# Optimization experiments

Measured on AMD Instinct MI355X. Metric: run time of the kernel, lower is better.

The kernel has to match this reference:

```python
import jax, jax.numpy as jnp
import numpy as np

B, T, D = 2, 4096, 1024
H, L = 8, 2
DH = D // H           # 128
BS = 64               # bucket_size (lucidrains default)
NH = 8                # n_hashes (lucidrains default)
NB = T // BS          # 64 buckets (even, required)
FF = 4 * D


def setup_inputs() -> dict:
    key = jax.random.key(0)
    ks = jax.random.split(key, 16)
    s = 0.02
    return {
        'x': jax.random.normal(ks[0], (B, T, D), jnp.float32),
        'Wqk': jax.random.normal(ks[1], (L, D, H * DH), jnp.float32) * s,
        'Wv': jax.random.normal(ks[2], (L, D, H * DH), jnp.float32) * s,
        'Wout': jax.random.normal(ks[3], (L, H * DH, D), jnp.float32) * s,
        'bout': jnp.zeros((L, D), jnp.float32),
        'ln1_g': jnp.ones((L, D), jnp.float32),
        'ln1_b': jnp.zeros((L, D), jnp.float32),
        'W1': jax.random.normal(ks[4], (L, D, FF), jnp.float32) * s,
        'b1': jnp.zeros((L, FF), jnp.float32),
        'W2': jax.random.normal(ks[5], (L, FF, D), jnp.float32) * s,
        'b2': jnp.zeros((L, D), jnp.float32),
        'ln2_g': jnp.ones((L, D), jnp.float32),
        'ln2_b': jnp.zeros((L, D), jnp.float32),
        'rotations': jax.random.normal(ks[6], (L, DH, NH, NB // 2), jnp.float32),
    }


def _layer_norm(x, g, b):
    m = jnp.mean(x, axis=-1, keepdims=True)
    v = jnp.var(x, axis=-1, keepdims=True)
    return (x - m) * jax.lax.rsqrt(v + 1e-5) * g + b


def _look_one_back(x):
    # concat each chunk with the previous chunk (wrap-around), along the within-chunk axis
    return jnp.concatenate([x, jnp.roll(x, 1, axis=1)], axis=2)


def _lsh_attention(qk, v, rot):
    # qk, v: (bh, T, DH); rot: (DH, NH, NB//2). Causal LSH attention (lucidrains defaults).
    bh, t, d = qk.shape
    rotated = jnp.einsum('btd,dhr->bhtr', qk, rot)
    rotated = jnp.concatenate([rotated, -rotated], axis=-1)          # (bh, NH, T, NB)
    buckets = jnp.argmax(rotated, axis=-1)                            # (bh, NH, T)
    buckets = buckets + (jnp.arange(NH) * NB)[None, :, None]
    buckets = buckets.reshape(bh, NH * t)
    ticker = jnp.arange(NH * t)
    buckets_and_t = buckets * t + (ticker % t)
    sticker = jnp.argsort(buckets_and_t, axis=-1)                     # stable
    undo_sort = jnp.argsort(sticker, axis=-1)
    st = sticker % t                                                  # original positions
    sqk = jnp.take_along_axis(qk, st[..., None], axis=1)              # (bh, NH*T, DH)
    sv = jnp.take_along_axis(v, st[..., None], axis=1)
    n_chunks = NH * NB
    bq = sqk.reshape(bh, n_chunks, BS, d)
    norm = jnp.maximum(jnp.linalg.norm(sqk, axis=-1, keepdims=True), 1e-12)
    bk = (sqk / norm).reshape(bh, n_chunks, BS, d)
    bv = sv.reshape(bh, n_chunks, BS, d)
    bk = _look_one_back(bk)                                           # (bh, nc, 2*BS, d)
    bv = _look_one_back(bv)
    dots = jnp.einsum('bcie,bcje->bcij', bq, bk) * (d ** -0.5)
    bq_t = st.reshape(bh, n_chunks, BS)
    bkv_t = _look_one_back(bq_t[..., None] * jnp.ones((1,), st.dtype))[..., 0] if False else jnp.concatenate([bq_t, jnp.roll(bq_t, 1, axis=1)], axis=2)
    causal = bq_t[:, :, :, None] < bkv_t[:, :, None, :]
    dots = jnp.where(causal, -1e9, dots)
    self_mask = bq_t[:, :, :, None] == bkv_t[:, :, None, :]
    dots = jnp.where(self_mask, -5e4, dots)                           # TOKEN_SELF_ATTN_VALUE
    lse = jax.scipy.special.logsumexp(dots, axis=-1, keepdims=True)
    p = jnp.exp(dots - lse)
    bo = jnp.einsum('bcij,bcje->bcie', p, bv)
    so = bo.reshape(bh, NH * t, d)
    o = jnp.take_along_axis(so, undo_sort[..., None], axis=1)
    logits = jnp.take_along_axis(lse.reshape(bh, NH * t), undo_sort, axis=1)
    o = o.reshape(bh, NH, t, d)
    logits = logits.reshape(bh, NH, t, 1)
    probs = jnp.exp(logits - jax.scipy.special.logsumexp(logits, axis=1, keepdims=True))
    return jnp.sum(o * probs, axis=1)                                 # (bh, T, DH)


def _attn_block(x, Wqk, Wv, Wout, bout, g, b, rot):
    h = _layer_norm(x, g, b)
    qk = (h @ Wqk).reshape(B, T, H, DH).transpose(0, 2, 1, 3).reshape(B * H, T, DH)
    v = (h @ Wv).reshape(B, T, H, DH).transpose(0, 2, 1, 3).reshape(B * H, T, DH)
    o = _lsh_attention(qk, v, rot)
    o = o.reshape(B, H, T, DH).transpose(0, 2, 1, 3).reshape(B, T, H * DH)
    return o @ Wout + bout


def _ff_block(x, W1, b1, W2, b2, g, b):
    h = _layer_norm(x, g, b)
    return jax.nn.gelu(h @ W1 + b1, approximate=False) @ W2 + b2


def reference(x, Wqk, Wv, Wout, bout, ln1_g, ln1_b, W1, b1, W2, b2, ln2_g, ln2_b, rotations):
    # Reversible Reformer: x duplicated into two streams
    x1, x2 = x, x
    for l in range(L):
        x1 = x1 + _attn_block(x2, Wqk[l], Wv[l], Wout[l], bout[l], ln1_g[l], ln1_b[l], rotations[l])
        x2 = x2 + _ff_block(x1, W1[l], b1[l], W2[l], b2[l], ln2_g[l], ln2_b[l])
    out = (x1 + x2) * 0.5
    # mean-pool over sequence, reshape (1, B, D)
    return jnp.mean(out, axis=1).reshape(1, -1, D)
```

## Files before the change

kernel.cpp:

```cpp
#include <hip/hip_runtime.h>
#include <hip/hip_bf16.h>
#include <stdint.h>

#define B_ 2
#define T_ 4096
#define D_ 1024
#define H_ 8
#define DH_ 128
#define L_ 2
#define BS_ 64
#define NH_ 8
#define NB_ 64
#define NC_ (NH_*NB_)
#define FF_ 4096
#define BH_ (B_*H_)

typedef __hip_bfloat16 bf16;
typedef __attribute__((ext_vector_type(8))) short short8;
typedef __attribute__((ext_vector_type(4))) float f32x4;

typedef __attribute__((address_space(3))) uint32_t lds_u32_t;
typedef const __attribute__((address_space(1))) uint32_t glb_u32_t;

__device__ __forceinline__ void async_load16(const void* g, void* l) {
  __builtin_amdgcn_global_load_lds((glb_u32_t*)g, (lds_u32_t*)l, 16, 0, 0);
}

__global__ void diag_kernel(float* __restrict__ out, float a, float b) {
  if (threadIdx.x == 0) { out[0] = a; out[1] = b; }
}

__global__ void copy2_kernel(const float* __restrict__ x, float* __restrict__ x1,
                             float* __restrict__ x2) {
  int idx = blockIdx.x * 256 + threadIdx.x;
  if (idx < B_ * T_ * D_ / 4) {
    float4 v = ((const float4*)x)[idx];
    ((float4*)x1)[idx] = v;
    ((float4*)x2)[idx] = v;
  }
}

__global__ __launch_bounds__(256)
void transpose_cvt(const float* __restrict__ src, bf16* __restrict__ dst, int K, int N) {
  __shared__ float tile[32][33];
  const int n0 = blockIdx.x * 32, k0 = blockIdx.y * 32;
  const int c = threadIdx.x & 31, r8 = threadIdx.x >> 5;
#pragma unroll
  for (int i = 0; i < 32; i += 8) tile[r8 + i][c] = src[(size_t)(k0 + r8 + i) * N + n0 + c];
  __syncthreads();
#pragma unroll
  for (int i = 0; i < 32; i += 8)
    dst[(size_t)(n0 + r8 + i) * K + k0 + c] = __float2bfloat16(tile[c][r8 + i]);
}

__global__ __launch_bounds__(256)
void ln_kernel(const float* __restrict__ x, const float* __restrict__ g,
               const float* __restrict__ b, bf16* __restrict__ h) {
  __shared__ float red[8];
  const int row = blockIdx.x;
  const float* xr = x + (size_t)row * D_;
  const int tid = threadIdx.x;
  float4 xv = *(const float4*)(xr + tid * 4);
  float vals[4] = {xv.x, xv.y, xv.z, xv.w};
  float s = vals[0] + vals[1] + vals[2] + vals[3];
  float s2 = vals[0]*vals[0] + vals[1]*vals[1] + vals[2]*vals[2] + vals[3]*vals[3];
#pragma unroll
  for (int o = 1; o < 64; o <<= 1) { s += __shfl_xor(s, o, 64); s2 += __shfl_xor(s2, o, 64); }
  const int w = tid >> 6, lane = tid & 63;
  if (lane == 0) { red[w] = s; red[4 + w] = s2; }
  __syncthreads();
  s = red[0] + red[1] + red[2] + red[3];
  s2 = red[4] + red[5] + red[6] + red[7];
  const float mean = s * (1.0f / D_);
  const float var = s2 * (1.0f / D_) - mean * mean;
  const float rstd = rsqrtf(var + 1e-5f);
  bf16* hr = h + (size_t)row * D_;
#pragma unroll
  for (int i = 0; i < 4; ++i) {
    const int c = tid * 4 + i;
    hr[c] = __float2bfloat16((vals[i] - mean) * rstd * g[c] + b[c]);
  }
}

template<int EPI>
__global__ __launch_bounds__(512)
void gemm_bt_k(const bf16* __restrict__ A, const bf16* __restrict__ Bt,
               void* __restrict__ dst, const float* __restrict__ bias,
               float* __restrict__ resid, int M, int N, int K) {
  __shared__ __align__(16) bf16 sA[2][128 * 64];
  __shared__ __align__(16) bf16 sB[2][128 * 64];
  const int tid = threadIdx.x;

  const int GX = gridDim.x;
  const int nwg = GX * gridDim.y;
  const int orig = blockIdx.y * GX + blockIdx.x;
  int m0, n0;
  if ((nwg & 7) == 0 && (gridDim.y & 7) == 0) {
    const int cpx = nwg >> 3;
    const int lin = (orig & 7) * cpx + (orig >> 3);
    const int gsz = GX << 3;
    const int group = lin / gsz;
    const int rem = lin - group * gsz;
    m0 = ((group << 3) + (rem & 7)) << 7;
    n0 = (rem >> 3) << 7;
  } else {
    m0 = blockIdx.y << 7;
    n0 = blockIdx.x << 7;
  }

  const int lane = tid & 63;
  const int wv = tid >> 6;
  const int wm = (wv >> 2) << 6;
  const int wn = (wv & 3) << 5;
  const int l15 = lane & 15, lq = lane >> 4;

  f32x4 acc[4][2];
#pragma unroll
  for (int i = 0; i < 4; ++i)
#pragma unroll
    for (int j = 0; j < 2; ++j) acc[i][j] = (f32x4){0.f, 0.f, 0.f, 0.f};

  const bf16* Ab = A + (size_t)m0 * K;
  const bf16* Bb = Bt + (size_t)n0 * K;

  const int r0s = tid >> 3, ch0 = tid & 7;
  const int r1s = r0s + 64;
  const size_t sa0 = (size_t)r0s * K + (size_t)((ch0 ^ (r0s & 7)) << 3);
  const size_t sa1 = (size_t)r1s * K + (size_t)((ch0 ^ (r1s & 7)) << 3);

  auto stage = [&](int t) {
    const int b = t & 1;
    const size_t ko = (size_t)t << 6;
    async_load16(Ab + sa0 + ko, (char*)sA[b] + tid * 16);
    async_load16(Ab + sa1 + ko, (char*)sA[b] + (tid + 512) * 16);
    async_load16(Bb + sa0 + ko, (char*)sB[b] + tid * 16);
    async_load16(Bb + sa1 + ko, (char*)sB[b] + (tid + 512) * 16);
  };

  auto compute = [&](int b) {
    const bf16* __restrict__ pA = sA[b];
    const bf16* __restrict__ pB = sB[b];
#pragma unroll
    for (int kk = 0; kk < 2; ++kk) {
      short8 af[4], bfr[2];
#pragma unroll
      for (int mi = 0; mi < 4; ++mi) {
        const int row = wm + mi * 16 + l15;
        const int chunk = (kk * 4 + lq) ^ (row & 7);
        af[mi] = *(const short8*)(pA + (row << 6) + (chunk << 3));
      }
#pragma unroll
      for (int ni = 0; ni < 2; ++ni) {
        const int row = wn + ni * 16 + l15;
        const int chunk = (kk * 4 + lq) ^ (row & 7);
        bfr[ni] = *(const short8*)(pB + (row << 6) + (chunk << 3));
      }
#pragma unroll
      for (int mi = 0; mi < 4; ++mi)
#pragma unroll
        for (int ni = 0; ni < 2; ++ni)
          acc[mi][ni] = __builtin_amdgcn_mfma_f32_16x16x32_bf16(af[mi], bfr[ni], acc[mi][ni], 0, 0, 0);
    }
  };

  stage(0);
  __syncthreads();
  const int NT = K >> 6;
  for (int t = 0; t < NT; ++t) {
    if (t + 1 < NT) stage(t + 1);
    compute(t & 1);
    if (t + 1 < NT) __syncthreads();
  }

  const int cr = lq << 2;
#pragma unroll
  for (int mi = 0; mi < 4; ++mi) {
#pragma unroll
    for (int ni = 0; ni < 2; ++ni) {
#pragma unroll
      for (int j = 0; j < 4; ++j) {
        const int r = m0 + wm + mi * 16 + cr + j;
        const int c = n0 + wn + ni * 16 + l15;
        float val = acc[mi][ni][j];
        if (EPI == 0) {
          const int bb = r >> 12, t2 = r & (T_ - 1);
          const int hh = c >> 7, dh = c & (DH_ - 1);
          ((bf16*)dst)[(((size_t)(bb * H_ + hh)) * T_ + t2) * DH_ + dh] = __float2bfloat16(val);
        } else if (EPI == 2) {
          resid[(size_t)r * N + c] += val + bias[c];
        } else if (EPI == 3) {
          const float xg = val + bias[c];
          ((bf16*)dst)[(size_t)r * N + c] =
              __float2bfloat16(0.5f * xg * (1.0f + erff(xg * 0.70710678118654752440f)));
        } else if (EPI == 4) {
          ((bf16*)dst)[(size_t)r * N + c] = __float2bfloat16(val);
        }
      }
    }
  }
}

__global__ void bucket_kernel(const bf16* __restrict__ rotv, uint8_t* __restrict__ buckets) {
  const int idx = blockIdx.x * 256 + threadIdx.x;
  if (idx >= BH_ * T_ * NH_) return;
  const int row = idx >> 3, hh = idx & 7;
  const bf16* p = rotv + (size_t)row * 256 + hh * 32;
  float vmax = -3e38f, vmin = 3e38f;
  int imax = 0, imin = 0;
  for (int r = 0; r < 32; ++r) {
    const float xv = __bfloat162float(p[r]);
    if (xv > vmax) { vmax = xv; imax = r; }
    if (xv < vmin) { vmin = xv; imin = r; }
  }
  const int bkt = (vmax >= -vmin) ? imax : 32 + imin;
  const int bh = row >> 12, t = row & (T_ - 1);
  buckets[((size_t)(bh * 8 + hh) << 12) + t] = (uint8_t)bkt;
}

__global__ __launch_bounds__(256)
void sort_kernel(const uint8_t* __restrict__ buckets, int* __restrict__ st,
                 int* __restrict__ inv) {
  __shared__ uint8_t bk[T_];
  __shared__ int wsum[4];
  const int tid = threadIdx.x;
  const int grp = blockIdx.x;
  const uint8_t* src = buckets + (size_t)grp * T_;
  int* dst = st + (size_t)grp * T_;
  int* ivd = inv ? inv + (size_t)grp * T_ : nullptr;
  for (int i = tid; i < T_; i += 256) bk[i] = src[i];
  __syncthreads();
  const int lane = tid & 63, w = tid >> 6;
  const int t0 = tid * 16;
  int base = 0;
  for (int b = 0; b < 64; ++b) {
    int cnt = 0;
#pragma unroll
    for (int j = 0; j < 16; ++j) cnt += (bk[t0 + j] == b) ? 1 : 0;
    int incl = cnt;
    for (int o = 1; o < 64; o <<= 1) {
      int vv = __shfl_up(incl, o, 64);
      if (lane >= o) incl += vv;
    }
    if (lane == 63) wsum[w] = incl;
    __syncthreads();
    int wo = 0;
    for (int i = 0; i < w; ++i) wo += wsum[i];
    const int tot = wsum[0] + wsum[1] + wsum[2] + wsum[3];
    int pos = base + wo + incl - cnt;
    for (int j = 0; j < 16; ++j)
      if (bk[t0 + j] == b) {
        dst[pos] = t0 + j;
        if (ivd) ivd[t0 + j] = pos;
        ++pos;
      }
    base += tot;
    __syncthreads();
  }
}

__global__ __launch_bounds__(256)
void qknorm_kernel(const bf16* __restrict__ qk, bf16* __restrict__ qkn,
                   float* __restrict__ qnorm) {
  const int wid = (blockIdx.x * 256 + threadIdx.x) >> 6;
  const int lane = threadIdx.x & 63;
  if (wid >= BH_ * T_) return;
  const bf16* src = qk + (size_t)wid * DH_;
  const float a = __bfloat162float(src[2 * lane]);
  const float b = __bfloat162float(src[2 * lane + 1]);
  float ss = a * a + b * b;
#pragma unroll
  for (int o = 1; o < 64; o <<= 1) ss += __shfl_xor(ss, o, 64);
  const float nrm = sqrtf(ss);
  const float sc = 1.0f / fmaxf(nrm, 1e-12f);
  bf16* d = qkn + (size_t)wid * DH_;
  d[2 * lane] = __float2bfloat16(a * sc);
  d[2 * lane + 1] = __float2bfloat16(b * sc);
  if (lane == 0) qnorm[wid] = nrm;
}

__global__ __launch_bounds__(256)
void attn_sorted(const bf16* __restrict__ qkn, const float* __restrict__ qnormg,
                 const bf16* __restrict__ v, const int* __restrict__ st,
                 bf16* __restrict__ so, float* __restrict__ lseg) {
  __shared__ __align__(16) bf16 sK[128 * 136];
  __shared__ __align__(16) uint32_t sVT[128][68];
  __shared__ int stkv[128];
  __shared__ float snq[64];

  const int tid = threadIdx.x;
  const int cb = blockIdx.x;
  const int bh = blockIdx.y;
  const int hh = blockIdx.z;
  const int cg = hh * NB_ + cb;
  const int pg = (cg + NC_ - 1) & (NC_ - 1);
  const int* stb = st + (size_t)bh * (NH_ * T_);
  if (tid < 128) {
    const int p = (tid < 64) ? (cg * BS_ + tid) : (pg * BS_ + tid - 64);
    stkv[tid] = stb[p];
  }
  __syncthreads();

  const size_t vbase = (size_t)bh * T_ * DH_;
  if (tid < 64) snq[tid] = qnormg[(size_t)bh * T_ + stkv[tid]];
  {
    const int part = tid & 15, row = tid >> 4;
    for (int r0 = 0; r0 < 128; r0 += 16) {
      const int rr = r0 + row;
      const int t = stkv[rr];
      *(float4*)&sK[rr * 136 + part * 8] = *(const float4*)(qkn + vbase + (size_t)t * DH_ + part * 8);
    }
  }
  {
    for (int it = 0; it < 4; ++it) {
      const int idx = it * 256 + tid;
      const int g = idx & 15, kp = idx >> 4;
      const int t0 = stkv[2 * kp], t1 = stkv[2 * kp + 1];
      float4 a = *(const float4*)(v + vbase + (size_t)t0 * DH_ + g * 8);
      float4 b = *(const float4*)(v + vbase + (size_t)t1 * DH_ + g * 8);
      const unsigned short* ua = (const unsigned short*)&a;
      const unsigned short* ub = (const unsigned short*)&b;
      const int csw = (g & 7) << 2;
#pragma unroll
      for (int j = 0; j < 8; ++j)
        sVT[g * 8 + j][kp ^ csw] = (uint32_t)ua[j] | ((uint32_t)ub[j] << 16);
    }
  }
  __syncthreads();

  const int lane = tid & 63;
  const int w = tid >> 6;
  const int l15 = lane & 15, lq = lane >> 4;

  f32x4 acc[8];
#pragma unroll
  for (int i = 0; i < 8; ++i) acc[i] = (f32x4){0.f, 0.f, 0.f, 0.f};
#pragma unroll
  for (int kk = 0; kk < 4; ++kk) {
    short8 af = *(const short8*)&sK[(w * 16 + l15) * 136 + lq * 8 + kk * 32];
#pragma unroll
    for (int ni = 0; ni < 8; ++ni) {
      short8 bf = *(const short8*)&sK[(ni * 16 + l15) * 136 + lq * 8 + kk * 32];
      acc[ni] = __builtin_amdgcn_mfma_f32_16x16x32_bf16(af, bf, acc[ni], 0, 0, 0);
    }
  }
  __syncthreads();

  bf16* sP = sK;

  float lsev[4];
  const float scale = 0.08838834764831845f;
#pragma unroll
  for (int j = 0; j < 4; ++j) {
    const int row = w * 16 + lq * 4 + j;
    const int tq = stkv[row];
    const float rowsc = scale * snq[row];
    float mx = -3.0e38f;
#pragma unroll
    for (int ni = 0; ni < 8; ++ni) {
      const int tk = stkv[ni * 16 + l15];
      float val = acc[ni][j] * rowsc;
      if (tq < tk) val = -1e9f;
      else if (tq == tk) val = -5e4f;
      acc[ni][j] = val;
      mx = fmaxf(mx, val);
    }
#pragma unroll
    for (int o = 1; o < 16; o <<= 1) mx = fmaxf(mx, __shfl_xor(mx, o, 64));
    float se = 0.f;
#pragma unroll
    for (int ni = 0; ni < 8; ++ni) se += __expf(acc[ni][j] - mx);
#pragma unroll
    for (int o = 1; o < 16; o <<= 1) se += __shfl_xor(se, o, 64);
    const float inv = 1.0f / se;
#pragma unroll
    for (int ni = 0; ni < 8; ++ni)
      sP[row * 136 + ni * 16 + l15] = __float2bfloat16(__expf(acc[ni][j] - mx) * inv);
    lsev[j] = mx + __logf(se);
  }
  __syncthreads();

  f32x4 acc2[8];
#pragma unroll
  for (int i = 0; i < 8; ++i) acc2[i] = (f32x4){0.f, 0.f, 0.f, 0.f};
#pragma unroll
  for (int kk = 0; kk < 4; ++kk) {
    short8 pa = *(const short8*)&sP[(w * 16 + l15) * 136 + lq * 8 + kk * 32];
#pragma unroll
    for (int ni = 0; ni < 8; ++ni) {
      const int row = ni * 16 + l15;
      const int col = (lq * 4 + kk * 16) ^ (((row >> 3) & 7) << 2);
      short8 bv = *(const short8*)&sVT[row][col];
      acc2[ni] = __builtin_amdgcn_mfma_f32_16x16x32_bf16(pa, bv, acc2[ni], 0, 0, 0);
    }
  }

  const size_t sobase = ((size_t)(hh * BH_ + bh) * T_ + (size_t)cb * BS_) * DH_;
#pragma unroll
  for (int j = 0; j < 4; ++j) {
    const int row = w * 16 + lq * 4 + j;
    if (l15 == 0)
      lseg[(size_t)(hh * BH_ + bh) * T_ + cb * BS_ + row] = lsev[j];
    bf16* orow = so + sobase + (size_t)row * DH_;
#pragma unroll
    for (int ni = 0; ni < 8; ++ni)
      orow[ni * 16 + l15] = __float2bfloat16(acc2[ni][j]);
  }
}

__global__ __launch_bounds__(256)
void combine2_kernel(const bf16* __restrict__ so, const float* __restrict__ lseg,
                     const int* __restrict__ ipos, bf16* __restrict__ ocomb) {
  const int gw = (blockIdx.x * 256 + threadIdx.x) >> 6;
  const int lane = threadIdx.x & 63;
  if (gw >= BH_ * T_) return;
  const int bh = gw >> 12, t = gw & (T_ - 1);
  float lse8 = -3.0e38f;
  int p8 = 0;
  if (lane < 8) {
    p8 = ipos[((size_t)bh * NH_ + lane) * T_ + t];
    lse8 = lseg[((size_t)lane * BH_ + bh) * T_ + p8];
  }
  float m = -3.0e38f;
#pragma unroll
  for (int h = 0; h < 8; ++h) m = fmaxf(m, __shfl(lse8, h, 64));
  float s = 0.f;
#pragma unroll
  for (int h = 0; h < 8; ++h) s += __expf(__shfl(lse8, h, 64) - m);
  const float invs = 1.0f / s;
  float a0 = 0.f, a1 = 0.f;
#pragma unroll
  for (int h = 0; h < 8; ++h) {
    const int ph = __shfl(p8, h, 64);
    const float wh = __expf(__shfl(lse8, h, 64) - m) * invs;
    const bf16* rp = so + (((size_t)h * BH_ + bh) * T_ + ph) * DH_ + lane * 2;
    a0 += wh * __bfloat162float(rp[0]);
    a1 += wh * __bfloat162float(rp[1]);
  }
  const int bb = bh >> 3, hd = bh & 7;
  bf16* dp = ocomb + ((size_t)(bb * T_ + t)) * D_ + hd * DH_ + lane * 2;
  dp[0] = __float2bfloat16(a0);
  dp[1] = __float2bfloat16(a1);
}

__global__ __launch_bounds__(256)
void attn_kernel(const bf16* __restrict__ qkn, const float* __restrict__ qnormg,
                 const bf16* __restrict__ v, const int* __restrict__ st,
                 float* __restrict__ mg, float* __restrict__ sg,
                 float* __restrict__ oac, int hh) {
  __shared__ __align__(16) bf16 sK[128 * 136];
  __shared__ __align__(16) uint32_t sVT[128][68];
  __shared__ int stkv[128];
  __shared__ float snq[64];

  const int tid = threadIdx.x;
  const int cb = blockIdx.x;
  const int bh = blockIdx.y;
  const int cg = hh * NB_ + cb;
  const int pg = (cg + NC_ - 1) & (NC_ - 1);
  const int* stb = st + (size_t)bh * (NH_ * T_);
  if (tid < 128) {
    const int p = (tid < 64) ? (cg * BS_ + tid) : (pg * BS_ + tid - 64);
    stkv[tid] = stb[p];
  }
  __syncthreads();

  const size_t vbase = (size_t)bh * T_ * DH_;
  if (tid < 64) snq[tid] = qnormg[(size_t)bh * T_ + stkv[tid]];
  {
    const int part = tid & 15, row = tid >> 4;
    for (int r0 = 0; r0 < 128; r0 += 16) {
      const int rr = r0 + row;
      const int t = stkv[rr];
      *(float4*)&sK[rr * 136 + part * 8] = *(const float4*)(qkn + vbase + (size_t)t * DH_ + part * 8);
    }
  }
  {
    for (int it = 0; it < 4; ++it) {
      const int idx = it * 256 + tid;
      const int g = idx & 15, kp = idx >> 4;
      const int t0 = stkv[2 * kp], t1 = stkv[2 * kp + 1];
      float4 a = *(const float4*)(v + vbase + (size_t)t0 * DH_ + g * 8);
      float4 b = *(const float4*)(v + vbase + (size_t)t1 * DH_ + g * 8);
      const unsigned short* ua = (const unsigned short*)&a;
      const unsigned short* ub = (const unsigned short*)&b;
#pragma unroll
      for (int j = 0; j < 8; ++j)
        sVT[g * 8 + j][kp] = (uint32_t)ua[j] | ((uint32_t)ub[j] << 16);
    }
  }
  __syncthreads();

  const int lane = tid & 63;
  const int w = tid >> 6;
  const int l15 = lane & 15, lq = lane >> 4;

  f32x4 acc[8];
#pragma unroll
  for (int i = 0; i < 8; ++i) acc[i] = (f32x4){0.f, 0.f, 0.f, 0.f};
#pragma unroll
  for (int kk = 0; kk < 4; ++kk) {
    short8 af = *(const short8*)&sK[(w * 16 + l15) * 136 + lq * 8 + kk * 32];
#pragma unroll
    for (int ni = 0; ni < 8; ++ni) {
      short8 bf = *(const short8*)&sK[(ni * 16 + l15) * 136 + lq * 8 + kk * 32];
      acc[ni] = __builtin_amdgcn_mfma_f32_16x16x32_bf16(af, bf, acc[ni], 0, 0, 0);
    }
  }
  __syncthreads();

  bf16* sP = sK;

  float lsev[4];
  const float scale = 0.08838834764831845f;
#pragma unroll
  for (int j = 0; j < 4; ++j) {
    const int row = w * 16 + lq * 4 + j;
    const int tq = stkv[row];
    const float rowsc = scale * snq[row];
    float mx = -3.0e38f;
#pragma unroll
    for (int ni = 0; ni < 8; ++ni) {
      const int tk = stkv[ni * 16 + l15];
      float val = acc[ni][j] * rowsc;
      if (tq < tk) val = -1e9f;
      else if (tq == tk) val = -5e4f;
      acc[ni][j] = val;
      mx = fmaxf(mx, val);
    }
#pragma unroll
    for (int o = 1; o < 16; o <<= 1) mx = fmaxf(mx, __shfl_xor(mx, o, 64));
    float se = 0.f;
#pragma unroll
    for (int ni = 0; ni < 8; ++ni) se += __expf(acc[ni][j] - mx);
#pragma unroll
    for (int o = 1; o < 16; o <<= 1) se += __shfl_xor(se, o, 64);
    const float inv = 1.0f / se;
#pragma unroll
    for (int ni = 0; ni < 8; ++ni)
      sP[row * 136 + ni * 16 + l15] = __float2bfloat16(__expf(acc[ni][j] - mx) * inv);
    lsev[j] = mx + __logf(se);
  }
  __syncthreads();

  f32x4 acc2[8];
#pragma unroll
  for (int i = 0; i < 8; ++i) acc2[i] = (f32x4){0.f, 0.f, 0.f, 0.f};
#pragma unroll
  for (int kk = 0; kk < 4; ++kk) {
    short8 pa = *(const short8*)&sP[(w * 16 + l15) * 136 + lq * 8 + kk * 32];
#pragma unroll
    for (int ni = 0; ni < 8; ++ni) {
      short8 bv = *(const short8*)&sVT[ni * 16 + l15][lq * 4 + kk * 16];
      acc2[ni] = __builtin_amdgcn_mfma_f32_16x16x32_bf16(pa, bv, acc2[ni], 0, 0, 0);
    }
  }

#pragma unroll
  for (int j = 0; j < 4; ++j) {
    const int row = w * 16 + lq * 4 + j;
    const int t = stkv[row];
    const size_t gi = (size_t)bh * T_ + t;
    const float ls = lsev[j];
    float* orow = oac + gi * DH_;
    if (hh == 0) {
      if (l15 == 0) { sg[gi] = 1.0f; mg[gi] = ls; }
#pragma unroll
      for (int ni = 0; ni < 8; ++ni) orow[ni * 16 + l15] = acc2[ni][j];
    } else {
      const float mo = mg[gi];
      const float mn = fmaxf(mo, ls);
      const float al = __expf(mo - mn);
      const float be = __expf(ls - mn);
      if (l15 == 0) { sg[gi] = sg[gi] * al + be; mg[gi] = mn; }
#pragma unroll
      for (int ni = 0; ni < 8; ++ni) {
        const int c = ni * 16 + l15;
        orow[c] = orow[c] * al + be * acc2[ni][j];
      }
    }
  }
}

__global__ void combine_kernel(const float* __restrict__ oac, const float* __restrict__ sg,
                               bf16* __restrict__ ocomb) {
  const int idx = blockIdx.x * 256 + threadIdx.x;
  if (idx >= BH_ * T_ * DH_ / 4) return;
  const int rowtok = idx >> 5;
  const int gsub = idx & 31;
  const float inv = 1.0f / sg[rowtok];
  float4 ov = ((const float4*)oac)[idx];
  const int bh = rowtok >> 12, t = rowtok & (T_ - 1);
  const int bb = bh >> 3, hd = bh & 7;
  bf16* dp = ocomb + ((size_t)(bb * T_ + t)) * D_ + hd * DH_ + gsub * 4;
  dp[0] = __float2bfloat16(ov.x * inv);
  dp[1] = __float2bfloat16(ov.y * inv);
  dp[2] = __float2bfloat16(ov.z * inv);
  dp[3] = __float2bfloat16(ov.w * inv);
}

__global__ void pool_partial(const float* __restrict__ x1, const float* __restrict__ x2,
                             float* __restrict__ part) {
  const int b = blockIdx.y, slice = blockIdx.x;
  const int tid = threadIdx.x;
  float acc[4] = {0.f, 0.f, 0.f, 0.f};
  for (int r = 0; r < 32; ++r) {
    const size_t base = ((size_t)b * T_ + slice * 32 + r) * D_;
#pragma unroll
    for (int i = 0; i < 4; ++i) {
      const int c = tid + i * 256;
      acc[i] += x1[base + c] + x2[base + c];
    }
  }
#pragma unroll
  for (int i = 0; i < 4; ++i)
    part[((size_t)(b * 128 + slice)) * D_ + tid + i * 256] = acc[i];
}

__global__ void pool_reduce(const float* __restrict__ part, float* __restrict__ out) {
  const int idx = blockIdx.x * 256 + threadIdx.x;
  if (idx >= B_ * D_) return;
  const int b = idx >> 10, d = idx & 1023;
  float s = 0.f;
  for (int k = 0; k < 128; ++k) s += part[((size_t)(b * 128 + k)) * D_ + d];
  out[idx] = s * (0.5f / T_);
}

extern "C" void kernel_launch(void* const* d_in, const int* in_sizes, int n_in,
                              void* d_out, int out_size, void* d_ws, size_t ws_size,
                              hipStream_t stream) {
  (void)in_sizes; (void)n_in; (void)out_size;
  const float* x    = (const float*)d_in[0];
  const float* Wqk  = (const float*)d_in[1];
  const float* Wv   = (const float*)d_in[2];
  const float* Wout = (const float*)d_in[3];
  const float* bout = (const float*)d_in[4];
  const float* ln1g = (const float*)d_in[5];
  const float* ln1b = (const float*)d_in[6];
  const float* W1   = (const float*)d_in[7];
  const float* b1   = (const float*)d_in[8];
  const float* W2   = (const float*)d_in[9];
  const float* b2   = (const float*)d_in[10];
  const float* ln2g = (const float*)d_in[11];
  const float* ln2b = (const float*)d_in[12];
  const float* rot  = (const float*)d_in[13];
  float* out = (float*)d_out;

  char* ws = (char*)d_ws;
  const dim3 blk(256);
  const dim3 blk512(512);

  {
    size_t off = 0;
    auto alloc = [&](size_t b) { size_t o = off; off += (b + 255) & ~(size_t)255; return o; };
    const size_t o_x1  = alloc((size_t)B_ * T_ * D_ * 4);
    const size_t o_x2  = alloc((size_t)B_ * T_ * D_ * 4);
    const size_t o_hq  = alloc((size_t)B_ * T_ * D_ * 2);
    const size_t o_qk  = alloc((size_t)BH_ * T_ * DH_ * 2);
    const size_t o_vv  = alloc((size_t)BH_ * T_ * DH_ * 2);
    const size_t o_so  = alloc((size_t)NH_ * BH_ * T_ * DH_ * 2);
    const size_t o_lse = alloc((size_t)NH_ * BH_ * T_ * 4);
    const size_t o_st  = alloc((size_t)BH_ * NH_ * T_ * 4);
    const size_t o_ip  = alloc((size_t)BH_ * NH_ * T_ * 4);
    const size_t o_bkt = alloc((size_t)BH_ * NH_ * T_);
    const size_t o_qn  = alloc((size_t)BH_ * T_ * 4);
    const size_t o_part = alloc((size_t)B_ * 128 * D_ * 4);

    if (off <= ws_size) {
      float* x1   = (float*)(ws + o_x1);
      float* x2   = (float*)(ws + o_x2);
      bf16*  h    = (bf16*)(ws + o_hq);
      bf16*  qkn  = (bf16*)(ws + o_hq);
      bf16*  qk   = (bf16*)(ws + o_qk);
      bf16*  ocomb = (bf16*)(ws + o_qk);
      bf16*  vv   = (bf16*)(ws + o_vv);
      bf16*  so   = (bf16*)(ws + o_so);
      float* lse  = (float*)(ws + o_lse);
      int*   st   = (int*)(ws + o_st);
      int*   ip   = (int*)(ws + o_ip);
      uint8_t* bkt = (uint8_t*)(ws + o_bkt);
      float* qn   = (float*)(ws + o_qn);
      float* part = (float*)(ws + o_part);
      bf16* wqkT = (bf16*)(ws + o_so);
      bf16* wvT  = wqkT + (size_t)D_ * D_;
      bf16* rotT = wvT + (size_t)D_ * D_;
      bf16* rotd = (bf16*)(ws + o_so + ((size_t)16 << 20));
      bf16* woT  = (bf16*)(ws + o_so);
      bf16* ffh  = (bf16*)(ws + o_so);
      bf16* w1T  = (bf16*)(ws + o_so + ((size_t)64 << 20));
      bf16* w2T  = w1T + (size_t)D_ * FF_;

      copy2_kernel<<<dim3(B_ * T_ * D_ / 4 / 256), blk, 0, stream>>>(x, x1, x2);

      for (int l = 0; l < L_; ++l) {
        transpose_cvt<<<dim3(32, 32), blk, 0, stream>>>(Wqk + (size_t)l * D_ * D_, wqkT, D_, D_);
        transpose_cvt<<<dim3(32, 32), blk, 0, stream>>>(Wv + (size_t)l * D_ * D_, wvT, D_, D_);
        transpose_cvt<<<dim3(8, 4), blk, 0, stream>>>(rot + (size_t)l * DH_ * 256, rotT, DH_, 256);

        ln_kernel<<<dim3(B_ * T_), blk, 0, stream>>>(x2, ln1g + l * D_, ln1b + l * D_, h);
        gemm_bt_k<0><<<dim3(8, 64), blk512, 0, stream>>>(h, wqkT, qk, nullptr, nullptr, B_ * T_, D_, D_);
        gemm_bt_k<0><<<dim3(8, 64), blk512, 0, stream>>>(h, wvT, vv, nullptr, nullptr, B_ * T_, D_, D_);
        qknorm_kernel<<<dim3(BH_ * T_ / 4), blk, 0, stream>>>(qk, qkn, qn);
        gemm_bt_k<4><<<dim3(2, 512), blk512, 0, stream>>>(qkn, rotT, rotd, nullptr, nullptr, BH_ * T_, 256, DH_);
        bucket_kernel<<<dim3(BH_ * T_ * NH_ / 256), blk, 0, stream>>>(rotd, bkt);
        sort_kernel<<<dim3(BH_ * NH_), blk, 0, stream>>>(bkt, st, ip);
        attn_sorted<<<dim3(NB_, BH_, NH_), blk, 0, stream>>>(qkn, qn, vv, st, so, lse);
        combine2_kernel<<<dim3(BH_ * T_ / 4), blk, 0, stream>>>(so, lse, ip, ocomb);
        transpose_cvt<<<dim3(32, 32), blk, 0, stream>>>(Wout + (size_t)l * D_ * D_, woT, D_, D_);
        gemm_bt_k<2><<<dim3(8, 64), blk512, 0, stream>>>(ocomb, woT, nullptr, bout + l * D_, x1, B_ * T_, D_, D_);

        transpose_cvt<<<dim3(128, 32), blk, 0, stream>>>(W1 + (size_t)l * D_ * FF_, w1T, D_, FF_);
        transpose_cvt<<<dim3(32, 128), blk, 0, stream>>>(W2 + (size_t)l * FF_ * D_, w2T, FF_, D_);
        ln_kernel<<<dim3(B_ * T_), blk, 0, stream>>>(x1, ln2g + l * D_, ln2b + l * D_, h);
        gemm_bt_k<3><<<dim3(32, 64), blk512, 0, stream>>>(h, w1T, ffh, b1 + l * FF_, nullptr, B_ * T_, FF_, D_);
        gemm_bt_k<2><<<dim3(8, 64), blk512, 0, stream>>>(ffh, w2T, nullptr, b2 + l * D_, x2, B_ * T_, D_, FF_);
      }

      pool_partial<<<dim3(128, B_), blk, 0, stream>>>(x1, x2, part);
      pool_reduce<<<dim3((B_ * D_ + 255) / 256), blk, 0, stream>>>(part, out);
      return;
    }
  }

  size_t off = 0;
  auto alloc = [&](size_t b) { size_t o = off; off += (b + 255) & ~(size_t)255; return o; };
  const size_t o_x1   = alloc((size_t)B_ * T_ * D_ * 4);
  const size_t o_x2   = alloc((size_t)B_ * T_ * D_ * 4);
  const size_t o_hq   = alloc((size_t)B_ * T_ * D_ * 2);
  const size_t o_qk   = alloc((size_t)BH_ * T_ * DH_ * 2);
  const size_t o_vv   = alloc((size_t)BH_ * T_ * DH_ * 2);
  const size_t o_oac  = alloc((size_t)BH_ * T_ * DH_ * 4);
  const size_t o_st   = alloc((size_t)BH_ * NH_ * T_ * 4);
  const size_t o_bkt  = alloc((size_t)BH_ * NH_ * T_);
  const size_t o_mg   = alloc((size_t)BH_ * T_ * 4);
  const size_t o_sg   = alloc((size_t)BH_ * T_ * 4);
  const size_t o_qn   = alloc((size_t)BH_ * T_ * 4);
  const size_t o_part = alloc((size_t)B_ * 128 * D_ * 4);
  const size_t o_w    = alloc((size_t)D_ * FF_ * 2 * 2);
  if (off > ws_size) {
    diag_kernel<<<dim3(1), dim3(64), 0, stream>>>(out, (float)ws_size, (float)off);
    return;
  }

  float* x1   = (float*)(ws + o_x1);
  float* x2   = (float*)(ws + o_x2);
  bf16*  h    = (bf16*)(ws + o_hq);
  bf16*  qkn  = (bf16*)(ws + o_hq);
  bf16*  qk   = (bf16*)(ws + o_qk);
  bf16*  ocomb = (bf16*)(ws + o_qk);
  bf16*  vv   = (bf16*)(ws + o_vv);
  float* oac  = (float*)(ws + o_oac);
  bf16*  rotd = (bf16*)(ws + o_oac);
  bf16*  ffh  = (bf16*)(ws + o_qk);
  int*   st   = (int*)(ws + o_st);
  uint8_t* bkt = (uint8_t*)(ws + o_bkt);
  float* mg   = (float*)(ws + o_mg);
  float* sg   = (float*)(ws + o_sg);
  float* qn   = (float*)(ws + o_qn);
  float* part = (float*)(ws + o_part);
  bf16* wqkT = (bf16*)(ws + o_w);
  bf16* wvT  = (bf16*)(ws + o_w + (size_t)D_ * D_ * 2);
  bf16* woT  = (bf16*)(ws + o_w + (size_t)D_ * D_ * 2 * 2);
  bf16* rotT = (bf16*)(ws + o_w + (size_t)D_ * D_ * 2 * 3);
  bf16* w1T  = (bf16*)(ws + o_w);
  bf16* w2T  = (bf16*)(ws + o_w + (size_t)D_ * FF_ * 2);

  copy2_kernel<<<dim3(B_ * T_ * D_ / 4 / 256), blk, 0, stream>>>(x, x1, x2);

  for (int l = 0; l < L_; ++l) {
    transpose_cvt<<<dim3(32, 32), blk, 0, stream>>>(Wqk + (size_t)l * D_ * D_, wqkT, D_, D_);
    transpose_cvt<<<dim3(32, 32), blk, 0, stream>>>(Wv + (size_t)l * D_ * D_, wvT, D_, D_);
    transpose_cvt<<<dim3(32, 32), blk, 0, stream>>>(Wout + (size_t)l * D_ * D_, woT, D_, D_);
    transpose_cvt<<<dim3(8, 4), blk, 0, stream>>>(rot + (size_t)l * DH_ * 256, rotT, DH_, 256);

    ln_kernel<<<dim3(B_ * T_), blk, 0, stream>>>(x2, ln1g + l * D_, ln1b + l * D_, h);
    gemm_bt_k<0><<<dim3(8, 64), blk512, 0, stream>>>(h, wqkT, qk, nullptr, nullptr, B_ * T_, D_, D_);
    gemm_bt_k<0><<<dim3(8, 64), blk512, 0, stream>>>(h, wvT, vv, nullptr, nullptr, B_ * T_, D_, D_);
    qknorm_kernel<<<dim3(BH_ * T_ / 4), blk, 0, stream>>>(qk, qkn, qn);
    gemm_bt_k<4><<<dim3(2, 512), blk512, 0, stream>>>(qkn, rotT, rotd, nullptr, nullptr, BH_ * T_, 256, DH_);
    bucket_kernel<<<dim3(BH_ * T_ * NH_ / 256), blk, 0, stream>>>(rotd, bkt);
    sort_kernel<<<dim3(BH_ * NH_), blk, 0, stream>>>(bkt, st, nullptr);
    for (int hh = 0; hh < NH_; ++hh)
      attn_kernel<<<dim3(NB_, BH_), blk, 0, stream>>>(qkn, qn, vv, st, mg, sg, oac, hh);
    combine_kernel<<<dim3(BH_ * T_ * DH_ / 4 / 256), blk, 0, stream>>>(oac, sg, ocomb);
    gemm_bt_k<2><<<dim3(8, 64), blk512, 0, stream>>>(ocomb, woT, nullptr, bout + l * D_, x1, B_ * T_, D_, D_);

    transpose_cvt<<<dim3(128, 32), blk, 0, stream>>>(W1 + (size_t)l * D_ * FF_, w1T, D_, FF_);
    transpose_cvt<<<dim3(32, 128), blk, 0, stream>>>(W2 + (size_t)l * FF_ * D_, w2T, FF_, D_);

    ln_kernel<<<dim3(B_ * T_), blk, 0, stream>>>(x1, ln2g + l * D_, ln2b + l * D_, h);
    gemm_bt_k<3><<<dim3(32, 64), blk512, 0, stream>>>(h, w1T, ffh, b1 + l * FF_, nullptr, B_ * T_, FF_, D_);
    gemm_bt_k<2><<<dim3(8, 64), blk512, 0, stream>>>(ffh, w2T, nullptr, b2 + l * D_, x2, B_ * T_, D_, FF_);
  }

  pool_partial<<<dim3(128, B_), blk, 0, stream>>>(x1, x2, part);
  pool_reduce<<<dim3((B_ * D_ + 255) / 256), blk, 0, stream>>>(part, out);
}
```

Baseline: 1.186 ms.

## Fuse LSH bucket argmax into rotation GEMM epilogue; nontemporal attn output traffic

Adds a GEMM epilogue (EPI 5) that computes the argmax over the rotated and negated projections in registers, using cross-lane shuffles within each 32-column hash group, and writes the uint8 bucket ids directly. This removes the bf16 rotated-score intermediate and the separate bucket_kernel launch. The attention partial outputs are now written with nontemporal stores and read in the combine kernel with nontemporal loads, to reduce cache pollution. Risks: the argmax tie-breaking and rounding may differ from the old bf16-intermediate path, and the nontemporal hints may hurt if the combine reads would have hit in cache.

```diff
diff --git a/kernel.cpp b/kernel.cpp
--- a/kernel.cpp
+++ b/kernel.cpp
@@ -173,6 +173,35 @@
   }
 
   const int cr = lq << 2;
+  if (EPI == 5) {
+    const int hh2 = (n0 + wn) >> 5;
+#pragma unroll
+    for (int mi = 0; mi < 4; ++mi) {
+#pragma unroll
+      for (int j = 0; j < 4; ++j) {
+        const float v0 = acc[mi][0][j], v1 = acc[mi][1][j];
+        float bmx = v0; int imx = l15;
+        if (v1 > bmx) { bmx = v1; imx = 16 + l15; }
+        float bmn = v0; int imn = l15;
+        if (v1 < bmn) { bmn = v1; imn = 16 + l15; }
+#pragma unroll
+        for (int o = 1; o < 16; o <<= 1) {
+          const float ov = __shfl_xor(bmx, o, 64); const int oi = __shfl_xor(imx, o, 64);
+          if (ov > bmx || (ov == bmx && oi < imx)) { bmx = ov; imx = oi; }
+          const float ov2 = __shfl_xor(bmn, o, 64); const int oi2 = __shfl_xor(imn, o, 64);
+          if (ov2 < bmn || (ov2 == bmn && oi2 < imn)) { bmn = ov2; imn = oi2; }
+        }
+        if (l15 == 0) {
+          const int r = m0 + wm + mi * 16 + cr + j;
+          const int bh = r >> 12, t2 = r & (T_ - 1);
+          const int bkt = (bmx >= -bmn) ? imx : 32 + imn;
+          ((uint8_t*)dst)[((size_t)(bh * 8 + hh2) << 12) + t2] = (uint8_t)bkt;
+        }
+      }
+    }
+    return;
+  }
+
 #pragma unroll
   for (int mi = 0; mi < 4; ++mi) {
 #pragma unroll
@@ -402,8 +431,11 @@
       lseg[(size_t)(hh * BH_ + bh) * T_ + cb * BS_ + row] = lsev[j];
     bf16* orow = so + sobase + (size_t)row * DH_;
 #pragma unroll
-    for (int ni = 0; ni < 8; ++ni)
-      orow[ni * 16 + l15] = __float2bfloat16(acc2[ni][j]);
+    for (int ni = 0; ni < 8; ++ni) {
+      bf16 hv = __float2bfloat16(acc2[ni][j]);
+      __builtin_nontemporal_store(*(unsigned short*)&hv,
+                                  (unsigned short*)(orow + ni * 16 + l15));
+    }
   }
 }
 
@@ -432,9 +464,12 @@
   for (int h = 0; h < 8; ++h) {
     const int ph = __shfl(p8, h, 64);
     const float wh = __expf(__shfl(lse8, h, 64) - m) * invs;
-    const bf16* rp = so + (((size_t)h * BH_ + bh) * T_ + ph) * DH_ + lane * 2;
-    a0 += wh * __bfloat162float(rp[0]);
-    a1 += wh * __bfloat162float(rp[1]);
+    const unsigned short* rp =
+        (const unsigned short*)(so + (((size_t)h * BH_ + bh) * T_ + ph) * DH_ + lane * 2);
+    unsigned short u0 = __builtin_nontemporal_load(rp);
+    unsigned short u1 = __builtin_nontemporal_load(rp + 1);
+    a0 += wh * __bfloat162float(*(const bf16*)&u0);
+    a1 += wh * __bfloat162float(*(const bf16*)&u1);
   }
   const int bb = bh >> 3, hd = bh & 7;
   bf16* dp = ocomb + ((size_t)(bb * T_ + t)) * D_ + hd * DH_ + lane * 2;
@@ -683,7 +718,6 @@
       bf16* wqkT = (bf16*)(ws + o_so);
       bf16* wvT  = wqkT + (size_t)D_ * D_;
       bf16* rotT = wvT + (size_t)D_ * D_;
-      bf16* rotd = (bf16*)(ws + o_so + ((size_t)16 << 20));
       bf16* woT  = (bf16*)(ws + o_so);
       bf16* ffh  = (bf16*)(ws + o_so);
       bf16* w1T  = (bf16*)(ws + o_so + ((size_t)64 << 20));
@@ -700,8 +734,7 @@
         gemm_bt_k<0><<<dim3(8, 64), blk512, 0, stream>>>(h, wqkT, qk, nullptr, nullptr, B_ * T_, D_, D_);
         gemm_bt_k<0><<<dim3(8, 64), blk512, 0, stream>>>(h, wvT, vv, nullptr, nullptr, B_ * T_, D_, D_);
         qknorm_kernel<<<dim3(BH_ * T_ / 4), blk, 0, stream>>>(qk, qkn, qn);
-        gemm_bt_k<4><<<dim3(2, 512), blk512, 0, stream>>>(qkn, rotT, rotd, nullptr, nullptr, BH_ * T_, 256, DH_);
-        bucket_kernel<<<dim3(BH_ * T_ * NH_ / 256), blk, 0, stream>>>(rotd, bkt);
+        gemm_bt_k<5><<<dim3(2, 512), blk512, 0, stream>>>(qkn, rotT, bkt, nullptr, nullptr, BH_ * T_, 256, DH_);
         sort_kernel<<<dim3(BH_ * NH_), blk, 0, stream>>>(bkt, st, ip);
         attn_sorted<<<dim3(NB_, BH_, NH_), blk, 0, stream>>>(qkn, qn, vv, st, so, lse);
         combine2_kernel<<<dim3(BH_ * T_ / 4), blk, 0, stream>>>(so, lse, ip, ocomb);
```

Measured after the change: 1.195 ms. About the same (+0.8%).
